# Kernel optimization log

Hardware: AMD Instinct MI355X
Metric: run time of the kernel (lower is better)

## Reference

```python
import jax, jax.numpy as jnp
import numpy as np
from jax import lax

# LiteMSA config: in_ch=256, out_ch=256, dim=8, heads=32, total_dim=256, scales=(3,)
DIM = 8
QKV_CH = 768          # 3 * total_dim
PW_GROUPS = 96        # 3 * heads


def setup_inputs() -> dict:
    key = jax.random.key(0)
    ks = jax.random.split(key, 5)
    x = jax.random.normal(ks[0], (16, 256, 64, 64), jnp.float32)
    w_qkv = jax.random.normal(ks[1], (768, 256), jnp.float32) * 0.02      # 1x1 conv
    w_dw = jax.random.normal(ks[2], (768, 1, 3, 3), jnp.float32) * 0.02   # depthwise 3x3
    w_pw = jax.random.normal(ks[3], (768, 8, 1, 1), jnp.float32) * 0.02   # grouped 1x1, 96 groups
    w_proj = jax.random.normal(ks[4], (256, 512), jnp.float32) * 0.02     # 1x1 conv
    bn_gamma = jnp.ones((256,), jnp.float32)
    bn_beta = jnp.zeros((256,), jnp.float32)
    bn_mean = jnp.zeros((256,), jnp.float32)
    bn_var = jnp.ones((256,), jnp.float32)
    return {"x": x, "w_qkv": w_qkv, "w_dw": w_dw, "w_pw": w_pw, "w_proj": w_proj,
            "bn_gamma": bn_gamma, "bn_beta": bn_beta, "bn_mean": bn_mean, "bn_var": bn_var}


def reference(x, w_qkv, w_dw, w_pw, w_proj, bn_gamma, bn_beta, bn_mean, bn_var):
    B, _, H, W = x.shape
    dn = ("NCHW", "OIHW", "NCHW")
    # qkv 1x1 conv
    qkv = jnp.einsum("bchw,oc->bohw", x, w_qkv)  # [B,768,H,W]
    # multi-scale aggregation: depthwise 3x3 -> grouped 1x1
    agg = lax.conv_general_dilated(qkv, w_dw, (1, 1), "SAME",
                                   dimension_numbers=dn, feature_group_count=QKV_CH)
    agg = lax.conv_general_dilated(agg, w_pw, (1, 1), "SAME",
                                   dimension_numbers=dn, feature_group_count=PW_GROUPS)
    ms = jnp.concatenate([qkv, agg], axis=1)  # [B,1536,H,W]
    # [B, heads_total=64, N=H*W, 3*dim]
    ms = ms.reshape(B, -1, 3 * DIM, H * W).transpose(0, 1, 3, 2)
    q = jax.nn.relu(ms[..., :DIM])
    k = jax.nn.relu(ms[..., DIM:2 * DIM])
    v = ms[..., 2 * DIM:]
    # pad v with ones for normalizer channel
    v = jnp.concatenate([v, jnp.ones(v.shape[:-1] + (1,), v.dtype)], axis=-1)  # [B,h,N,dim+1]
    kv = jnp.einsum("bhnd,bhne->bhde", k, v)   # [B,h,dim,dim+1]
    out = jnp.einsum("bhnd,bhde->bhne", q, kv)  # [B,h,N,dim+1]
    out = out[..., :DIM] / (out[..., DIM:] + 1e-15)
    out = out.transpose(0, 1, 3, 2).reshape(B, -1, H, W)  # [B,512,H,W]
    # proj 1x1 conv + BatchNorm (inference, running stats)
    y = jnp.einsum("bchw,oc->bohw", out, w_proj)
    inv = bn_gamma / jnp.sqrt(bn_var + 1e-5)
    y = y * inv[None, :, None, None] + (bn_beta - bn_mean * inv)[None, :, None, None]
    return y
```

## Files before the change

kernel.cpp:

```cpp
#include <hip/hip_runtime.h>
#include <hip/hip_bf16.h>


#define NB 16
#define CQKV 768
#define P4096 4096
#define QFIX_CAP (1u << 21)

typedef __bf16 bf16x8 __attribute__((ext_vector_type(8)));
typedef float f32x4 __attribute__((ext_vector_type(4)));

#define MFMA_BF16 __builtin_amdgcn_mfma_f32_16x16x32_bf16

__device__ __forceinline__ ushort f2bf(float f) {
    union { float f; unsigned int u; } x; x.f = f;
    unsigned int u = x.u;
    unsigned int r = (u + 0x7FFFu + ((u >> 16) & 1u)) >> 16;
    return (ushort)r;
}
__device__ __forceinline__ float bf2f(ushort u) {
    union { unsigned int u; float f; } x; x.u = ((unsigned int)u) << 16;
    return x.f;
}
__device__ __forceinline__ unsigned int pk2bf(float x, float y) {
    __hip_bfloat162 h = __float22bfloat162_rn(make_float2(x, y));
    union { __hip_bfloat162 b; unsigned int u; } c; c.b = h; return c.u;
}

__device__ __forceinline__ void gload16(void* lds, const void* g) {
    __builtin_amdgcn_global_load_lds(
        (const __attribute__((address_space(1))) void*)g,
        (__attribute__((address_space(3))) void*)lds, 16, 0, 0);
}

__global__ __launch_bounds__(128) void conv_w(
    const float* __restrict__ W, ushort* __restrict__ Ah, ushort* __restrict__ Al)
{
    const int rv = blockIdx.x;
    const int t  = threadIdx.x;
    int phys;
    if (rv < 256) phys = (rv >> 3) * 24 + (rv & 7);
    else { int r2 = rv - 256; phys = (r2 >> 4) * 24 + 8 + (r2 & 15); }
    int c = t * 2;
    float w0 = W[(size_t)phys * 256 + c];
    float w1 = W[(size_t)phys * 256 + c + 1];
    unsigned int h = pk2bf(w0, w1);
    float f0 = __uint_as_float(h << 16);
    float f1 = __uint_as_float(h & 0xffff0000u);
    unsigned int l = pk2bf(w0 - f0, w1 - f1);
    int sl = ((c >> 3) & 3) ^ ((rv >> 1) & 3);
    int idx = (c & ~31) + sl * 8 + (c & 7);
    *(unsigned int*)&Ah[(size_t)rv * 256 + idx] = h;
    *(unsigned int*)&Al[(size_t)rv * 256 + idx] = l;
}

__global__ __launch_bounds__(256) void conv_wp(
    const float* __restrict__ W, ushort* __restrict__ Awp)
{
    const int m = blockIdx.x;
    const int t = threadIdx.x;
    int c = t * 2;
    float w0 = W[(size_t)m * 512 + c];
    float w1 = W[(size_t)m * 512 + c + 1];
    unsigned int h = pk2bf(w0, w1);
    int sl = ((c >> 3) & 3) ^ ((m >> 1) & 3);
    int idx = (c & ~31) + sl * 8 + (c & 7);
    *(unsigned int*)&Awp[(size_t)m * 512 + idx] = h;
}

__global__ __launch_bounds__(256) void conv_x(
    const float* __restrict__ X, ushort* __restrict__ XTh, ushort* __restrict__ XTl)
{
    const int pt = blockIdx.x;
    const int ct = blockIdx.y;
    const int b  = blockIdx.z;
    const int t  = threadIdx.x;
    const int p0 = pt * 64, c0 = ct * 64;

    __shared__ float tile[64][65];

    {
        int cr = t >> 2, pc = (t & 3) * 16;
        const float* xr = X + ((size_t)b * 256 + c0 + cr) * P4096 + p0 + pc;
        float4 v0 = *(const float4*)xr;
        float4 v1 = *(const float4*)(xr + 4);
        float4 v2 = *(const float4*)(xr + 8);
        float4 v3 = *(const float4*)(xr + 12);
        float* d = &tile[cr][pc];
        d[0]=v0.x; d[1]=v0.y; d[2]=v0.z; d[3]=v0.w;
        d[4]=v1.x; d[5]=v1.y; d[6]=v1.z; d[7]=v1.w;
        d[8]=v2.x; d[9]=v2.y; d[10]=v2.z; d[11]=v2.w;
        d[12]=v3.x; d[13]=v3.y; d[14]=v3.z; d[15]=v3.w;
    }
    __syncthreads();

    #pragma unroll
    for (int pass = 0; pass < 2; pass++) {
        int tp = t >> 2;
        int cc = (t & 3) + pass * 4;
        int p  = p0 + tp;
        float v[8];
        #pragma unroll
        for (int j = 0; j < 8; j++) v[j] = tile[cc * 8 + j][tp];
        union { unsigned int u[4]; uint4 q; } H, L;
        #pragma unroll
        for (int i = 0; i < 4; i++) {
            unsigned int h = pk2bf(v[2 * i], v[2 * i + 1]);
            H.u[i] = h;
            float f0 = __uint_as_float(h << 16);
            float f1 = __uint_as_float(h & 0xffff0000u);
            L.u[i] = pk2bf(v[2 * i] - f0, v[2 * i + 1] - f1);
        }
        int c = c0 + cc * 8;
        int sl = ((c >> 3) & 3) ^ ((p >> 1) & 3);
        size_t idx = ((size_t)b * P4096 + p) * 256 + (c & ~31) + sl * 8;
        *(uint4*)&XTh[idx] = H.q;
        *(uint4*)&XTl[idx] = L.q;
    }
}

__global__ void zero_cnt(unsigned int* qmeta) { if (threadIdx.x == 0) qmeta[0] = 0; }

__global__ __launch_bounds__(256, 2) void gemm_fused(
    const ushort* __restrict__ Ah, const ushort* __restrict__ Al,
    const ushort* __restrict__ Bh, const ushort* __restrict__ Bl,
    ushort* __restrict__ Cbf, float* __restrict__ qplane,
    unsigned int* __restrict__ qmeta)
{
    const int hw = blockIdx.x;
    const int lg = (hw & 7) * 384 + (hw >> 3);
    const int mt = lg % 6;
    const int rem = lg / 6;
    const int n0 = (rem & 31) * 128;
    const int b  = rem >> 5;
    const int t  = threadIdx.x;
    const int wave = t >> 6, lane = t & 63, quad = lane >> 4, l15 = lane & 15;
    const int wr = wave >> 1, wc = wave & 1;
    const int M0 = mt * 128;

    __shared__ __align__(16) ushort AsH[2][4096];
    __shared__ __align__(16) ushort AsL[2][4096];
    __shared__ __align__(16) ushort BsH[2][4096];
    __shared__ __align__(16) ushort BsL[2][4096];

    int aoff[4], boff[4];
    #pragma unroll
    for (int i = 0; i < 4; i++) {
        int ra = wr * 64 + i * 16 + l15;
        aoff[i] = ra * 64 + ((quad ^ ((ra >> 1) & 3)) << 4);
        int rb = wc * 64 + i * 16 + l15;
        boff[i] = rb * 64 + ((quad ^ ((rb >> 1) & 3)) << 4);
    }

    const int srow = t >> 2;
    const int schunk = (t & 3) * 8;
    const size_t abase = (size_t)(M0 + srow) * 256 + schunk;
    const size_t bbase = ((size_t)b * P4096 + n0 + srow) * 256 + schunk;
    const int ldsoff = wave * 1024;

    f32x4 acc[4][4];
    #pragma unroll
    for (int mi = 0; mi < 4; mi++)
        #pragma unroll
        for (int nj = 0; nj < 4; nj++)
            #pragma unroll
            for (int r = 0; r < 4; r++) acc[mi][nj][r] = 0.0f;

    if (mt < 2) {
        auto stageQ = [&](int d, int kw) {
            #pragma unroll
            for (int i = 0; i < 2; i++) {
                int lo = ldsoff + i * 4096;
                size_t so = (size_t)(i * 64) * 256 + (size_t)kw * 32;
                gload16((char*)AsH[d] + lo, Ah + abase + so);
                gload16((char*)AsL[d] + lo, Al + abase + so);
                gload16((char*)BsH[d] + lo, Bh + bbase + so);
                gload16((char*)BsL[d] + lo, Bl + bbase + so);
            }
        };
        stageQ(0, 0);
        for (int kw = 0; kw < 8; kw++) {
            int cur = kw & 1;
            if (kw < 7) {
                stageQ(cur ^ 1, kw + 1);
                asm volatile("s_waitcnt vmcnt(8)" ::: "memory");
            } else {
                asm volatile("s_waitcnt vmcnt(0)" ::: "memory");
            }
            __builtin_amdgcn_s_barrier();
            bf16x8 ah[4], al[4];
            #pragma unroll
            for (int mi = 0; mi < 4; mi++) {
                ah[mi] = *(const bf16x8*)((const char*)AsH[cur] + aoff[mi]);
                al[mi] = *(const bf16x8*)((const char*)AsL[cur] + aoff[mi]);
            }
            #pragma unroll
            for (int nj = 0; nj < 4; nj++) {
                bf16x8 bh = *(const bf16x8*)((const char*)BsH[cur] + boff[nj]);
                bf16x8 bl = *(const bf16x8*)((const char*)BsL[cur] + boff[nj]);
                #pragma unroll
                for (int mi = 0; mi < 4; mi++) {
                    acc[mi][nj] = MFMA_BF16(ah[mi], bh, acc[mi][nj], 0, 0, 0);
                    acc[mi][nj] = MFMA_BF16(al[mi], bh, acc[mi][nj], 0, 0, 0);
                    acc[mi][nj] = MFMA_BF16(ah[mi], bl, acc[mi][nj], 0, 0, 0);
                }
            }
            __builtin_amdgcn_s_barrier();
        }
        unsigned int* qlist = qmeta + 16;
        #pragma unroll
        for (int mi = 0; mi < 4; mi++)
            #pragma unroll
            for (int nj = 0; nj < 4; nj++)
                #pragma unroll
                for (int r = 0; r < 4; r++) {
                    int rv = M0 + wr * 64 + mi * 16 + quad * 4 + r;
                    int rp = (rv >> 3) * 24 + (rv & 7);
                    int col = n0 + wc * 64 + nj * 16 + l15;
                    float v = acc[mi][nj][r];
                    Cbf[((size_t)b * CQKV + rp) * P4096 + col] = f2bf(v);
                    qplane[((size_t)b * 256 + rv) * P4096 + col] = v;
                    if (fabsf(v) < 1e-4f) {
                        unsigned int idx = atomicAdd(qmeta, 1u);
                        if (idx < QFIX_CAP)
                            qlist[idx] = (unsigned int)(((b * 256 + rv) << 12) | col);
                    }
                }
    } else {
        auto stageKV = [&](int d, int kw) {
            #pragma unroll
            for (int i = 0; i < 2; i++) {
                int lo = ldsoff + i * 4096;
                size_t so = (size_t)(i * 64) * 256 + (size_t)kw * 32;
                gload16((char*)AsH[d] + lo, Ah + abase + so);
                gload16((char*)BsH[d] + lo, Bh + bbase + so);
            }
        };
        stageKV(0, 0);
        for (int kw = 0; kw < 8; kw++) {
            int cur = kw & 1;
            if (kw < 7) {
                stageKV(cur ^ 1, kw + 1);
                asm volatile("s_waitcnt vmcnt(4)" ::: "memory");
            } else {
                asm volatile("s_waitcnt vmcnt(0)" ::: "memory");
            }
            __builtin_amdgcn_s_barrier();
            bf16x8 ah[4];
            #pragma unroll
            for (int mi = 0; mi < 4; mi++)
                ah[mi] = *(const bf16x8*)((const char*)AsH[cur] + aoff[mi]);
            #pragma unroll
            for (int nj = 0; nj < 4; nj++) {
                bf16x8 bh = *(const bf16x8*)((const char*)BsH[cur] + boff[nj]);
                #pragma unroll
                for (int mi = 0; mi < 4; mi++)
                    acc[mi][nj] = MFMA_BF16(ah[mi], bh, acc[mi][nj], 0, 0, 0);
            }
            __builtin_amdgcn_s_barrier();
        }
        #pragma unroll
        for (int mi = 0; mi < 4; mi++)
            #pragma unroll
            for (int nj = 0; nj < 4; nj++)
                #pragma unroll
                for (int r = 0; r < 4; r++) {
                    int rv2 = (M0 - 256) + wr * 64 + mi * 16 + quad * 4 + r;
                    int rp = (rv2 >> 4) * 24 + 8 + (rv2 & 15);
                    int col = n0 + wc * 64 + nj * 16 + l15;
                    Cbf[((size_t)b * CQKV + rp) * P4096 + col] = f2bf(acc[mi][nj][r]);
                }
    }
}

__global__ __launch_bounds__(256) void qfix2_kernel(
    float* __restrict__ qplane, const float* __restrict__ w_qkv,
    const float* __restrict__ x, const unsigned int* __restrict__ qmeta)
{
    unsigned int n = qmeta[0];
    if (n > QFIX_CAP) n = QFIX_CAP;
    const unsigned int* list = qmeta + 16;
    const int wave = threadIdx.x >> 6, lane = threadIdx.x & 63;
    for (unsigned int e = blockIdx.x * 4 + wave; e < n; e += gridDim.x * 4) {
        unsigned int i = list[e];
        int p   = (int)(i & 4095);
        int qch = (int)((i >> 12) & 255);
        int b   = (int)(i >> 20);
        int row = (qch >> 3) * 24 + (qch & 7);
        const float* wr = w_qkv + (size_t)row * 256;
        const float* xr = x + (size_t)b * 256 * P4096 + p;
        double s = 0.0;
        #pragma unroll
        for (int j = 0; j < 4; j++) {
            int c = lane * 4 + j;
            s += (double)wr[c] * (double)xr[(size_t)c * P4096];
        }
        #pragma unroll
        for (int off = 32; off > 0; off >>= 1) s += __shfl_xor(s, off, 64);
        if (lane == 0)
            qplane[((size_t)(b * 256 + qch)) * P4096 + p] = (float)s;
    }
}

__global__ __launch_bounds__(512, 8) void dwpw_kernel(
    const ushort* __restrict__ qkv, const float* __restrict__ wdw,
    const float* __restrict__ wpw, ushort* __restrict__ agg)
{
    const int rt = blockIdx.x;
    const int g  = blockIdx.y;
    const int b  = blockIdx.z;
    const int t  = threadIdx.x;
    const int r0 = rt * 16;
    const int cg = g * 8;

    __shared__ __align__(16) ushort tile[8][18][80];

    const ushort* src = qkv + ((size_t)(b * CQKV + cg)) * P4096;

    if (t < 288) {
        int ch = t / 36;
        int rr = (t % 36) >> 1;
        int side = t & 1;
        *(uint4*)&tile[ch][rr][side * 72] = make_uint4(0, 0, 0, 0);
    }
    #pragma unroll
    for (int i = 0; i < 3; i++) {
        int id = t + i * 512;
        if (id < 1152) {
            int ch  = id / 144;
            int rem = id - ch * 144;
            int rr  = rem >> 3;
            int oct = (rem & 7) * 8;
            int grow = r0 - 1 + rr;
            uint4 v = make_uint4(0, 0, 0, 0);
            if (grow >= 0 && grow < 64)
                v = *(const uint4*)(src + (size_t)ch * P4096 + (size_t)grow * 64 + oct);
            *(uint4*)&tile[ch][rr][8 + oct] = v;
        }
    }
    __syncthreads();

    const int kc  = t & 31;
    const int row = t >> 5;
    const float* wdwg = wdw + (size_t)cg * 9;
    const float* wpwg = wpw + (size_t)cg * 8;

    float acc0[8], acc1[8];
    #pragma unroll
    for (int oi = 0; oi < 8; oi++) { acc0[oi] = 0.0f; acc1[oi] = 0.0f; }

    #pragma unroll
    for (int c = 0; c < 8; c++) {
        float dv0 = 0.0f, dv1 = 0.0f;
        #pragma unroll
        for (int dy = 0; dy < 3; dy++) {
            const ushort* rp = &tile[c][row + dy][2 * kc + 4];
            unsigned int u1 = *(const unsigned int*)(rp + 2);
            unsigned int u2 = *(const unsigned int*)(rp + 4);
            unsigned int u3 = *(const unsigned int*)(rp + 6);
            float xm1 = __uint_as_float(u1 & 0xffff0000u);
            float x0  = __uint_as_float(u2 << 16);
            float x1  = __uint_as_float(u2 & 0xffff0000u);
            float x2  = __uint_as_float(u3 << 16);
            float w0 = wdwg[c * 9 + dy * 3 + 0];
            float w1 = wdwg[c * 9 + dy * 3 + 1];
            float w2 = wdwg[c * 9 + dy * 3 + 2];
            dv0 = fmaf(w0, xm1, dv0); dv0 = fmaf(w1, x0, dv0); dv0 = fmaf(w2, x1, dv0);
            dv1 = fmaf(w0, x0,  dv1); dv1 = fmaf(w1, x1, dv1); dv1 = fmaf(w2, x2, dv1);
        }
        #pragma unroll
        for (int oi = 0; oi < 8; oi++) {
            float w = wpwg[oi * 8 + c];
            acc0[oi] = fmaf(w, dv0, acc0[oi]);
            acc1[oi] = fmaf(w, dv1, acc1[oi]);
        }
    }

    size_t obase = ((size_t)(b * CQKV + cg)) * P4096 + (size_t)(r0 + row) * 64 + 2 * kc;
    #pragma unroll
    for (int oi = 0; oi < 8; oi++) {
        unsigned int u = (unsigned int)f2bf(acc0[oi]) |
                         ((unsigned int)f2bf(acc1[oi]) << 16);
        *(unsigned int*)&agg[obase + (size_t)oi * P4096] = u;
    }
}

__global__ __launch_bounds__(256) void kv_kernel(
    const ushort* __restrict__ qkv, const ushort* __restrict__ agg,
    float* __restrict__ kv)
{
    const int h = blockIdx.x, b = blockIdx.y, t = threadIdx.x;
    const ushort* src = (h < 32)
        ? qkv + ((size_t)(b * CQKV + h * 24)) * P4096
        : agg + ((size_t)(b * CQKV + (h - 32) * 24)) * P4096;

    float acc[72];
    #pragma unroll
    for (int i = 0; i < 72; i++) acc[i] = 0.0f;

    for (int pi = 0; pi < 16; pi++) {
        int p = t + pi * 256;
        float kvv[8], vv[8];
        #pragma unroll
        for (int d = 0; d < 8; d++) {
            float xk = bf2f(src[(size_t)(8 + d) * P4096 + p]);
            kvv[d] = xk > 0.0f ? xk : 0.0f;
        }
        #pragma unroll
        for (int e = 0; e < 8; e++) vv[e] = bf2f(src[(size_t)(16 + e) * P4096 + p]);
        #pragma unroll
        for (int d = 0; d < 8; d++) {
            #pragma unroll
            for (int e = 0; e < 8; e++) acc[d * 9 + e] += kvv[d] * vv[e];
            acc[d * 9 + 8] += kvv[d];
        }
    }

    #pragma unroll
    for (int i = 0; i < 72; i++) {
        float v = acc[i];
        #pragma unroll
        for (int off = 32; off > 0; off >>= 1) v += __shfl_xor(v, off, 64);
        acc[i] = v;
    }
    __shared__ float part[4][72];
    int wave = t >> 6, lane = t & 63;
    if (lane == 0) {
        #pragma unroll
        for (int i = 0; i < 72; i++) part[wave][i] = acc[i];
    }
    __syncthreads();
    if (t < 72)
        kv[((size_t)b * 64 + h) * 72 + t] = part[0][t] + part[1][t] + part[2][t] + part[3][t];
}

__global__ __launch_bounds__(256) void attn_out_kernel(
    const float* __restrict__ qplane, ushort* __restrict__ agg,
    const float* __restrict__ kv)
{
    const int pt = blockIdx.x, h = blockIdx.y, b = blockIdx.z, t = threadIdx.x;
    __shared__ float kvs[72];
    if (t < 72) kvs[t] = kv[((size_t)b * 64 + h) * 72 + t];
    __syncthreads();

    const bool lohead = (h < 32);
    const float* srcf = lohead
        ? qplane + ((size_t)(b * 256 + h * 8)) * P4096 : nullptr;
    const ushort* srcb = lohead ? nullptr
        : agg + ((size_t)(b * CQKV + (h - 32) * 24)) * P4096;

    int p = pt * 256 + t;
    float num[8]; float den = 0.0f;
    #pragma unroll
    for (int e = 0; e < 8; e++) num[e] = 0.0f;
    #pragma unroll
    for (int d = 0; d < 8; d++) {
        float q = lohead ? srcf[(size_t)d * P4096 + p]
                         : bf2f(srcb[(size_t)d * P4096 + p]);
        q = q > 0.0f ? q : 0.0f;
        #pragma unroll
        for (int e = 0; e < 8; e++) num[e] += q * kvs[d * 9 + e];
        den += q * kvs[d * 9 + 8];
    }
    float rd = 1.0f / (den + 1e-15f);
    ushort* dst = agg + ((size_t)(b * CQKV + (h / 2) * 24 + 8 + (h % 2) * 8)) * P4096 + p;
    #pragma unroll
    for (int e = 0; e < 8; e++)
        dst[(size_t)e * P4096] = f2bf(num[e] * rd);
}

__global__ __launch_bounds__(256, 2) void gemm_proj(
    const ushort* __restrict__ Awp,
    const ushort* __restrict__ Bagg,
    float* __restrict__ Y,
    const float* __restrict__ bn_g, const float* __restrict__ bn_b,
    const float* __restrict__ bn_m, const float* __restrict__ bn_v)
{
    const int hw = blockIdx.x;
    const int lg = (hw & 7) * 128 + (hw >> 3);
    const int mt = lg & 1;
    const int rem = lg >> 1;
    const int n0 = (rem & 31) * 128;
    const int b  = rem >> 5;
    const int t  = threadIdx.x;
    const int wave = t >> 6, lane = t & 63, quad = lane >> 4, l15 = lane & 15;
    const int wr = wave >> 1, wc = wave & 1;
    const int M0 = mt * 128;

    __shared__ __align__(16) ushort As[2][4096];
    __shared__ __align__(16) ushort Bs[2][5120];

    int aoff[4], boff[4];
    #pragma unroll
    for (int i = 0; i < 4; i++) {
        int ra = wr * 64 + i * 16 + l15;
        aoff[i] = ra * 64 + ((quad ^ ((ra >> 1) & 3)) << 4);
        int rb = wc * 64 + i * 16 + l15;
        boff[i] = rb * 80 + quad * 16;
    }

    const int arow0 = t >> 2, achk = (t & 3) * 8;
    const size_t abase = (size_t)(M0 + arow0) * 512 + achk;
    const size_t abase1 = (size_t)(M0 + 64 + arow0) * 512 + achk;
    const int ldsoffA = wave * 1024;

    const int bn_ = t & 127, half = t >> 7;
    const size_t bchanstride = (size_t)P4096;

    f32x4 acc[4][4];
    #pragma unroll
    for (int mi = 0; mi < 4; mi++)
        #pragma unroll
        for (int nj = 0; nj < 4; nj++)
            #pragma unroll
            for (int r = 0; r < 4; r++) acc[mi][nj][r] = 0.0f;

    auto stageA = [&](int d, int kw) {
        gload16((char*)As[d] + ldsoffA,        Awp + abase  + (size_t)kw * 32);
        gload16((char*)As[d] + ldsoffA + 4096, Awp + abase1 + (size_t)kw * 32);
    };
    ushort bu[16];
    auto loadB = [&](int kw) {
        const ushort* bsrc = Bagg
            + ((size_t)b * CQKV + (size_t)(kw * 2 + half) * 24 + 8) * P4096
            + n0 + bn_;
        #pragma unroll
        for (int j = 0; j < 16; j++) bu[j] = bsrc[(size_t)j * bchanstride];
    };
    auto writeB = [&](int d) {
        union { ushort us[8]; uint4 q; } P0, P1;
        #pragma unroll
        for (int j = 0; j < 8; j++) { P0.us[j] = bu[j]; P1.us[j] = bu[8 + j]; }
        ushort* dst = &Bs[d][bn_ * 40 + half * 16];
        *(uint4*)dst = P0.q;
        *(uint4*)(dst + 8) = P1.q;
    };

    stageA(0, 0);
    loadB(0);
    asm volatile("s_waitcnt vmcnt(0)" ::: "memory");
    writeB(0);
    asm volatile("s_waitcnt lgkmcnt(0)" ::: "memory");
    __builtin_amdgcn_s_barrier();

    for (int kw = 0; kw < 16; kw++) {
        int cur = kw & 1;
        if (kw < 15) {
            stageA(cur ^ 1, kw + 1);
            loadB(kw + 1);
        }
        bf16x8 af[4];
        #pragma unroll
        for (int mi = 0; mi < 4; mi++)
            af[mi] = *(const bf16x8*)((const char*)As[cur] + aoff[mi]);
        #pragma unroll
        for (int nj = 0; nj < 4; nj++) {
            bf16x8 bf = *(const bf16x8*)((const char*)Bs[cur] + boff[nj]);
            #pragma unroll
            for (int mi = 0; mi < 4; mi++)
                acc[mi][nj] = MFMA_BF16(af[mi], bf, acc[mi][nj], 0, 0, 0);
        }
        __builtin_amdgcn_s_barrier();
        if (kw < 15) {
            asm volatile("s_waitcnt vmcnt(0)" ::: "memory");
            writeB(cur ^ 1);
            asm volatile("s_waitcnt lgkmcnt(0)" ::: "memory");
        }
        __builtin_amdgcn_s_barrier();
    }

    #pragma unroll
    for (int mi = 0; mi < 4; mi++)
        #pragma unroll
        for (int nj = 0; nj < 4; nj++)
            #pragma unroll
            for (int r = 0; r < 4; r++) {
                int row = M0 + wr * 64 + mi * 16 + quad * 4 + r;
                int col = n0 + wc * 64 + nj * 16 + l15;
                float inv = bn_g[row] / sqrtf(bn_v[row] + 1e-5f);
                float v = acc[mi][nj][r] * inv + (bn_b[row] - bn_m[row] * inv);
                Y[((size_t)b * 256 + row) * P4096 + col] = v;
            }
}

extern "C" void kernel_launch(void* const* d_in, const int* in_sizes, int n_in,
                              void* d_out, int out_size, void* d_ws, size_t ws_size,
                              hipStream_t stream) {
    const float* x      = (const float*)d_in[0];
    const float* w_qkv  = (const float*)d_in[1];
    const float* w_dw   = (const float*)d_in[2];
    const float* w_pw   = (const float*)d_in[3];
    const float* w_proj = (const float*)d_in[4];
    const float* bn_g   = (const float*)d_in[5];
    const float* bn_b   = (const float*)d_in[6];
    const float* bn_m   = (const float*)d_in[7];
    const float* bn_v   = (const float*)d_in[8];
    float* y = (float*)d_out;

    char* ws = (char*)d_ws;
    ushort* qkv_bf = (ushort*)(ws);
    float*  qplane = (float*) (ws + 100663296);
    ushort* agg_bf = (ushort*)(ws + 167772160);
    ushort* XTh = (ushort*)(ws + 167772160);
    ushort* XTl = (ushort*)(ws + 167772160 + 33554432);
    ushort* Awh = (ushort*)(ws + 167772160 + 67108864);
    ushort* Awl = (ushort*)(ws + 167772160 + 67108864 + 393216);
    ushort* Awp = (ushort*)(ws + 100663296);
    float*  kvbuf  = (float*)d_out;
    unsigned int* qmeta = (unsigned int*)((char*)d_out + 524288);

    conv_w<<<dim3(768), 128, 0, stream>>>(w_qkv, Awh, Awl);
    zero_cnt<<<1, 64, 0, stream>>>(qmeta);
    conv_x<<<dim3(64, 4, NB), 256, 0, stream>>>(x, XTh, XTl);

    gemm_fused<<<dim3(3072), 256, 0, stream>>>(
        Awh, Awl, XTh, XTl, qkv_bf, qplane, qmeta);

    qfix2_kernel<<<dim3(1024), 256, 0, stream>>>(qplane, w_qkv, x, qmeta);

    dwpw_kernel<<<dim3(4, 96, NB), 512, 0, stream>>>(qkv_bf, w_dw, w_pw, agg_bf);

    kv_kernel<<<dim3(64, NB), 256, 0, stream>>>(qkv_bf, agg_bf, kvbuf);

    attn_out_kernel<<<dim3(16, 64, NB), 256, 0, stream>>>(qplane, agg_bf, kvbuf);

    conv_wp<<<dim3(256), 256, 0, stream>>>(w_proj, Awp);

    gemm_proj<<<dim3(1024), 256, 0, stream>>>(
        Awp, agg_bf, y, bn_g, bn_b, bn_m, bn_v);
}
```

Before: 396.6 us.

## Shrink gemm LDS for 3 blocks/CU, vectorize attn_out, fold counter reset

```diff
diff --git a/kernel.cpp b/kernel.cpp
--- a/kernel.cpp
+++ b/kernel.cpp
@@ -34,10 +34,12 @@
 }
 
 __global__ __launch_bounds__(128) void conv_w(
-    const float* __restrict__ W, ushort* __restrict__ Ah, ushort* __restrict__ Al)
+    const float* __restrict__ W, ushort* __restrict__ Ah, ushort* __restrict__ Al,
+    unsigned int* __restrict__ qmeta)
 {
     const int rv = blockIdx.x;
     const int t  = threadIdx.x;
+    if (rv == 0 && t == 0) qmeta[0] = 0;
     int phys;
     if (rv < 256) phys = (rv >> 3) * 24 + (rv & 7);
     else { int r2 = rv - 256; phys = (r2 >> 4) * 24 + 8 + (r2 & 15); }
@@ -119,9 +121,7 @@
     }
 }
 
-__global__ void zero_cnt(unsigned int* qmeta) { if (threadIdx.x == 0) qmeta[0] = 0; }
-
-__global__ __launch_bounds__(256, 2) void gemm_fused(
+__global__ __launch_bounds__(256, 3) void gemm_fused(
     const ushort* __restrict__ Ah, const ushort* __restrict__ Al,
     const ushort* __restrict__ Bh, const ushort* __restrict__ Bl,
     ushort* __restrict__ Cbf, float* __restrict__ qplane,
@@ -138,10 +138,7 @@
     const int wr = wave >> 1, wc = wave & 1;
     const int M0 = mt * 128;
 
-    __shared__ __align__(16) ushort AsH[2][4096];
-    __shared__ __align__(16) ushort AsL[2][4096];
-    __shared__ __align__(16) ushort BsH[2][4096];
-    __shared__ __align__(16) ushort BsL[2][4096];
+    __shared__ __align__(16) char smem[49152];
 
     int aoff[4], boff[4];
     #pragma unroll
@@ -167,37 +164,48 @@
             for (int r = 0; r < 4; r++) acc[mi][nj][r] = 0.0f;
 
     if (mt < 2) {
-        auto stageQ = [&](int d, int kw) {
+        char* AsH = smem;
+        char* AsL = smem + 8192;
+        char* BsH[2] = { smem + 16384, smem + 24576 };
+        char* BsL[2] = { smem + 32768, smem + 40960 };
+
+        auto stageA = [&](int kw) {
             #pragma unroll
             for (int i = 0; i < 2; i++) {
                 int lo = ldsoff + i * 4096;
                 size_t so = (size_t)(i * 64) * 256 + (size_t)kw * 32;
-                gload16((char*)AsH[d] + lo, Ah + abase + so);
-                gload16((char*)AsL[d] + lo, Al + abase + so);
-                gload16((char*)BsH[d] + lo, Bh + bbase + so);
-                gload16((char*)BsL[d] + lo, Bl + bbase + so);
+                gload16(AsH + lo, Ah + abase + so);
+                gload16(AsL + lo, Al + abase + so);
             }
         };
-        stageQ(0, 0);
+        auto stageB = [&](int d, int kw) {
+            #pragma unroll
+            for (int i = 0; i < 2; i++) {
+                int lo = ldsoff + i * 4096;
+                size_t so = (size_t)(i * 64) * 256 + (size_t)kw * 32;
+                gload16(BsH[d] + lo, Bh + bbase + so);
+                gload16(BsL[d] + lo, Bl + bbase + so);
+            }
+        };
+        stageA(0); stageB(0, 0);
         for (int kw = 0; kw < 8; kw++) {
             int cur = kw & 1;
-            if (kw < 7) {
-                stageQ(cur ^ 1, kw + 1);
-                asm volatile("s_waitcnt vmcnt(8)" ::: "memory");
-            } else {
-                asm volatile("s_waitcnt vmcnt(0)" ::: "memory");
-            }
+            asm volatile("s_waitcnt vmcnt(0)" ::: "memory");
             __builtin_amdgcn_s_barrier();
             bf16x8 ah[4], al[4];
             #pragma unroll
             for (int mi = 0; mi < 4; mi++) {
-                ah[mi] = *(const bf16x8*)((const char*)AsH[cur] + aoff[mi]);
-                al[mi] = *(const bf16x8*)((const char*)AsL[cur] + aoff[mi]);
-            }
+                ah[mi] = *(const bf16x8*)(AsH + aoff[mi]);
+                al[mi] = *(const bf16x8*)(AsL + aoff[mi]);
+            }
+            asm volatile("s_waitcnt lgkmcnt(0)" ::: "memory");
+            __builtin_amdgcn_sched_barrier(0);
+            __builtin_amdgcn_s_barrier();
+            if (kw < 7) { stageA(kw + 1); stageB(cur ^ 1, kw + 1); }
             #pragma unroll
             for (int nj = 0; nj < 4; nj++) {
-                bf16x8 bh = *(const bf16x8*)((const char*)BsH[cur] + boff[nj]);
-                bf16x8 bl = *(const bf16x8*)((const char*)BsL[cur] + boff[nj]);
+                bf16x8 bh = *(const bf16x8*)(BsH[cur] + boff[nj]);
+                bf16x8 bl = *(const bf16x8*)(BsL[cur] + boff[nj]);
                 #pragma unroll
                 for (int mi = 0; mi < 4; mi++) {
                     acc[mi][nj] = MFMA_BF16(ah[mi], bh, acc[mi][nj], 0, 0, 0);
@@ -205,7 +213,6 @@
                     acc[mi][nj] = MFMA_BF16(ah[mi], bl, acc[mi][nj], 0, 0, 0);
                 }
             }
-            __builtin_amdgcn_s_barrier();
         }
         unsigned int* qlist = qmeta + 16;
         #pragma unroll
@@ -227,13 +234,15 @@
                     }
                 }
     } else {
+        char* As[2] = { smem, smem + 8192 };
+        char* Bs[2] = { smem + 16384, smem + 24576 };
         auto stageKV = [&](int d, int kw) {
             #pragma unroll
             for (int i = 0; i < 2; i++) {
                 int lo = ldsoff + i * 4096;
                 size_t so = (size_t)(i * 64) * 256 + (size_t)kw * 32;
-                gload16((char*)AsH[d] + lo, Ah + abase + so);
-                gload16((char*)BsH[d] + lo, Bh + bbase + so);
+                gload16(As[d] + lo, Ah + abase + so);
+                gload16(Bs[d] + lo, Bh + bbase + so);
             }
         };
         stageKV(0, 0);
@@ -249,10 +258,10 @@
             bf16x8 ah[4];
             #pragma unroll
             for (int mi = 0; mi < 4; mi++)
-                ah[mi] = *(const bf16x8*)((const char*)AsH[cur] + aoff[mi]);
+                ah[mi] = *(const bf16x8*)(As[cur] + aoff[mi]);
             #pragma unroll
             for (int nj = 0; nj < 4; nj++) {
-                bf16x8 bh = *(const bf16x8*)((const char*)BsH[cur] + boff[nj]);
+                bf16x8 bh = *(const bf16x8*)(Bs[cur] + boff[nj]);
                 #pragma unroll
                 for (int mi = 0; mi < 4; mi++)
                     acc[mi][nj] = MFMA_BF16(ah[mi], bh, acc[mi][nj], 0, 0, 0);
@@ -449,24 +458,39 @@
     const ushort* srcb = lohead ? nullptr
         : agg + ((size_t)(b * CQKV + (h - 32) * 24)) * P4096;
 
-    int p = pt * 256 + t;
-    float num[8]; float den = 0.0f;
-    #pragma unroll
-    for (int e = 0; e < 8; e++) num[e] = 0.0f;
+    int p = pt * 512 + t * 2;
+    float num0[8], num1[8]; float den0 = 0.0f, den1 = 0.0f;
+    #pragma unroll
+    for (int e = 0; e < 8; e++) { num0[e] = 0.0f; num1[e] = 0.0f; }
     #pragma unroll
     for (int d = 0; d < 8; d++) {
-        float q = lohead ? srcf[(size_t)d * P4096 + p]
-                         : bf2f(srcb[(size_t)d * P4096 + p]);
-        q = q > 0.0f ? q : 0.0f;
-        #pragma unroll
-        for (int e = 0; e < 8; e++) num[e] += q * kvs[d * 9 + e];
-        den += q * kvs[d * 9 + 8];
-    }
-    float rd = 1.0f / (den + 1e-15f);
+        float q0, q1;
+        if (lohead) {
+            float2 qq = *(const float2*)(srcf + (size_t)d * P4096 + p);
+            q0 = qq.x; q1 = qq.y;
+        } else {
+            unsigned int u = *(const unsigned int*)(srcb + (size_t)d * P4096 + p);
+            q0 = bf2f((ushort)(u & 0xffff)); q1 = bf2f((ushort)(u >> 16));
+        }
+        q0 = q0 > 0.0f ? q0 : 0.0f;
+        q1 = q1 > 0.0f ? q1 : 0.0f;
+        #pragma unroll
+        for (int e = 0; e < 8; e++) {
+            num0[e] += q0 * kvs[d * 9 + e];
+            num1[e] += q1 * kvs[d * 9 + e];
+        }
+        den0 += q0 * kvs[d * 9 + 8];
+        den1 += q1 * kvs[d * 9 + 8];
+    }
+    float rd0 = 1.0f / (den0 + 1e-15f);
+    float rd1 = 1.0f / (den1 + 1e-15f);
     ushort* dst = agg + ((size_t)(b * CQKV + (h / 2) * 24 + 8 + (h % 2) * 8)) * P4096 + p;
     #pragma unroll
-    for (int e = 0; e < 8; e++)
-        dst[(size_t)e * P4096] = f2bf(num[e] * rd);
+    for (int e = 0; e < 8; e++) {
+        unsigned int u = (unsigned int)f2bf(num0[e] * rd0) |
+                         ((unsigned int)f2bf(num1[e] * rd1) << 16);
+        *(unsigned int*)(dst + (size_t)e * P4096) = u;
+    }
 }
 
 __global__ __launch_bounds__(256, 2) void gemm_proj(
@@ -609,8 +633,7 @@
     float*  kvbuf  = (float*)d_out;
     unsigned int* qmeta = (unsigned int*)((char*)d_out + 524288);
 
-    conv_w<<<dim3(768), 128, 0, stream>>>(w_qkv, Awh, Awl);
-    zero_cnt<<<1, 64, 0, stream>>>(qmeta);
+    conv_w<<<dim3(768), 128, 0, stream>>>(w_qkv, Awh, Awl, qmeta);
     conv_x<<<dim3(64, 4, NB), 256, 0, stream>>>(x, XTh, XTl);
 
     gemm_fused<<<dim3(3072), 256, 0, stream>>>(
@@ -622,7 +645,7 @@
 
     kv_kernel<<<dim3(64, NB), 256, 0, stream>>>(qkv_bf, agg_bf, kvbuf);
 
-    attn_out_kernel<<<dim3(16, 64, NB), 256, 0, stream>>>(qplane, agg_bf, kvbuf);
+    attn_out_kernel<<<dim3(8, 64, NB), 256, 0, stream>>>(qplane, agg_bf, kvbuf);
 
     conv_wp<<<dim3(256), 256, 0, stream>>>(w_proj, Awp);
 
```

After: 385.8 us. 1.03x faster.
